# Optimization experiments

Measured on AMD Instinct MI355X. Metric: run time of the kernel, lower is better.

The kernel has to match this reference:

```python
import jax, jax.numpy as jnp
import numpy as np

B = 32; SEQ = 900; GRID = 30; PFX = 16; D = 512
H = 8; HD = 64; WS = 3; SS = 1
NW = (GRID // WS) ** 2; N = WS * WS
INTER = 1536  # find_multiple(round(4.0*512*2/3), 256)
EPS = 1e-5
SCALE = HD ** -0.5


def _rel_pos_index():
    coords = np.stack(np.meshgrid(np.arange(WS), np.arange(WS), indexing='ij')).reshape(2, -1)
    rel = (coords[:, :, None] - coords[:, None, :]).transpose(1, 2, 0).copy()
    rel[:, :, 0] += WS - 1
    rel[:, :, 1] += WS - 1
    rel[:, :, 0] *= 2 * WS - 1
    return rel.sum(-1)  # [N, N]


def _attn_mask():
    img = np.zeros((GRID, GRID))
    cnt = 0
    sl = (slice(0, -WS), slice(-WS, -SS), slice(-SS, None))
    for h in sl:
        for w in sl:
            img[h, w] = cnt
            cnt += 1
    mw = img.reshape(GRID // WS, WS, GRID // WS, WS).transpose(0, 2, 1, 3).reshape(-1, N)
    diff = mw[:, None, :] - mw[:, :, None]
    return np.where(diff != 0, -100.0, 0.0).astype(np.float32)  # [nW, N, N]


REL_IDX = _rel_pos_index()
MASK = _attn_mask()


def rms_norm(x):
    xf = x.astype(jnp.float32)
    v = jnp.mean(xf * xf, -1, keepdims=True)
    return (xf * jax.lax.rsqrt(v + EPS)).astype(x.dtype)


def swiglu(x, gu_w, down_w):
    gu = x @ gu_w.T
    gate, up = gu[..., :INTER], gu[..., INTER:]
    return (jax.nn.silu(gate) * up) @ down_w.T


def setup_inputs() -> dict:
    key = jax.random.key(0)
    ks = jax.random.split(key, 8)
    s = 0.02
    return {
        'hidden_states': jax.random.normal(ks[0], (B, PFX + SEQ, D), jnp.float32),
        'qkv_w': jax.random.normal(ks[1], (3 * D, D), jnp.float32) * s,
        'qkv_b': jnp.zeros((3 * D,), jnp.float32),
        'proj_w': jax.random.normal(ks[2], (D, D), jnp.float32) * s,
        'proj_b': jnp.zeros((D,), jnp.float32),
        'rel_bias': jax.random.normal(ks[3], ((2 * WS - 1) ** 2, H), jnp.float32) * s,
        'gu_w': jax.random.normal(ks[4], (2 * INTER, D), jnp.float32) * s,
        'down_w': jax.random.normal(ks[5], (D, INTER), jnp.float32) * s,
        'pgu_w': jax.random.normal(ks[6], (2 * INTER, D), jnp.float32) * s,
        'pdown_w': jax.random.normal(ks[7], (D, INTER), jnp.float32) * s,
    }


def reference(hidden_states, qkv_w, qkv_b, proj_w, proj_b, rel_bias, gu_w, down_w, pgu_w, pdown_w):
    hs = hidden_states
    prefix = hs[:, :PFX]                                     # [B, 16, D]
    grid = hs[:, PFX:] + jnp.mean(prefix, 1, keepdims=True)  # broadcast prefix mean
    x = grid.reshape(B, GRID, GRID, D)
    residual = x
    # cyclic shift
    x = jnp.roll(x, (-SS, -SS), (1, 2))
    # window partition -> [B*nW, N, D]
    xw = x.reshape(B, GRID // WS, WS, GRID // WS, WS, D).transpose(0, 1, 3, 2, 4, 5).reshape(B * NW, N, D)
    qkv = (xw @ qkv_w.T + qkv_b).reshape(B * NW, N, 3, H, HD).transpose(2, 0, 3, 1, 4)
    q, k, v = qkv[0] * SCALE, qkv[1], qkv[2]                 # [B*nW, H, N, HD]
    attn = jnp.einsum('whid,whjd->whij', q, k)
    bias = rel_bias[jnp.asarray(REL_IDX).reshape(-1)].reshape(N, N, H).transpose(2, 0, 1)
    attn = attn + bias[None]
    attn = attn.reshape(B, NW, H, N, N) + jnp.asarray(MASK)[None, :, None]
    attn = jax.nn.softmax(attn.reshape(B * NW, H, N, N), -1)
    out = jnp.einsum('whij,whjd->whid', attn, v).transpose(0, 2, 1, 3).reshape(B * NW, N, D)
    out = out @ proj_w.T + proj_b
    # window reverse + reverse shift
    x = out.reshape(B, GRID // WS, GRID // WS, WS, WS, D).transpose(0, 1, 3, 2, 4, 5).reshape(B, GRID, GRID, D)
    x = jnp.roll(x, (SS, SS), (1, 2))
    x = rms_norm(residual.reshape(B, SEQ, D) + x.reshape(B, SEQ, D))
    prefix = rms_norm(prefix + swiglu(prefix, pgu_w, pdown_w))
    hs = jnp.concatenate([prefix, x], 1)
    return rms_norm(hs + swiglu(hs, gu_w, down_w))
```

## Files before the change

### kernel.cpp

```cpp
#include <hip/hip_runtime.h>
#include <cstdint>
#include <cstddef>

typedef float f32x4 __attribute__((ext_vector_type(4)));
typedef short s16x8 __attribute__((ext_vector_type(8)));
typedef short s16x4 __attribute__((ext_vector_type(4)));

#define DEV static __device__ __forceinline__

DEV float bf2f(short s) {
  union { unsigned u; float f; } c;
  c.u = ((unsigned)(unsigned short)s) << 16;
  return c.f;
}
DEV short f2bf(float f) {
  union { float f; unsigned u; } c;
  c.f = f;
  unsigned r = c.u + 0x7fffu + ((c.u >> 16) & 1u);
  return (short)(r >> 16);
}
DEV float wave_allsum(float v) {
#pragma unroll
  for (int off = 32; off > 0; off >>= 1) v += __shfl_xor(v, off, 64);
  return v;
}
DEV void gload_lds16(const void* g, void* l) {
  __builtin_amdgcn_global_load_lds(
      (const __attribute__((address_space(1))) void*)g,
      (__attribute__((address_space(3))) void*)l, 16, 0, 0);
}
DEV float silu_f(float g) { return g / (1.f + __expf(-g)); }

DEV int xcd_swizzle(int orig, int nwg) {
  int q = nwg >> 3, r = nwg & 7;
  int xcd = orig & 7, pos = orig >> 3;
  return (xcd < r ? xcd * (q + 1) : r * (q + 1) + (xcd - r) * q) + pos;
}

DEV void sync_phase() {
  asm volatile("s_waitcnt vmcnt(0)" ::: "memory");
  __builtin_amdgcn_s_barrier();
  __builtin_amdgcn_sched_barrier(0);
}

enum { EPI_BF16 = 0, EPI_BIAS_BF16 = 1, EPI_SCATTER = 4, EPI_ADDOUT = 5, EPI_GU = 6 };

template <int EPI>
__global__ __launch_bounds__(512, 2) void gemm8(
    const short* __restrict__ A, const short* __restrict__ W,
    const float* __restrict__ bias, void* __restrict__ outp,
    int M, int N, int K)
{
  __shared__ short lds[65536];
  const int tid = threadIdx.x;
  const int wid = tid >> 6, lane = tid & 63;
  const int wr = wid >> 2, wc = wid & 3;
  const int nwg = gridDim.x * gridDim.y;
  const int orig = blockIdx.y * gridDim.x + blockIdx.x;
  const int wg = xcd_swizzle(orig, nwg);
  const int bx = wg % gridDim.x, by = wg / gridDim.x;
  const int row0 = by * 256;
  const int c0 = bx * 256;

  f32x4 acc[8][4];
#pragma unroll
  for (int m = 0; m < 8; ++m)
#pragma unroll
    for (int n = 0; n < 4; ++n) acc[m][n] = f32x4{0.f, 0.f, 0.f, 0.f};

  const int srow = tid >> 3;
  const int k8s = (tid & 7) ^ (srow & 7);
  const short* aub[4];
  const short* bub[4];
#pragma unroll
  for (int u = 0; u < 4; ++u) {
    aub[u] = A + (size_t)(row0 + u * 64 + srow) * K + k8s * 8;
    bub[u] = W + (size_t)(c0 + u * 64 + srow) * K + k8s * 8;
  }
  const int ldw = wid * 512;

#define SA(d, u, kt) gload_lds16(aub[u] + (kt), &lds[(d)*16384 + (u)*4096 + ldw])
#define SB(d, u, kt) gload_lds16(bub[u] + (kt), &lds[32768 + (d)*16384 + (u)*4096 + ldw])
#define GATE(VN)                                              \
  asm volatile("s_waitcnt vmcnt(" #VN ")" ::: "memory");      \
  __builtin_amdgcn_s_barrier();                               \
  __builtin_amdgcn_sched_barrier(0);

  const int kg0 = (lane >> 4) ^ (lane & 7);
  const int kg1 = (4 + (lane >> 4)) ^ (lane & 7);
  const int aoff = (wr * 128 + (lane & 15)) * 64;
  const int boff = 32768 + (wc * 64 + (lane & 15)) * 64;

#define READ_B(d)                                                              \
  _Pragma("unroll") for (int n = 0; n < 4; ++n) {                              \
    bfr[0][n] = *(const s16x8*)&lds[(d)*16384 + boff + n * 1024 + kg0 * 8];    \
    bfr[1][n] = *(const s16x8*)&lds[(d)*16384 + boff + n * 1024 + kg1 * 8];    \
  }
#define DO_PHASE(d, p)                                                         \
  do {                                                                         \
    s16x8 a00 = *(const s16x8*)&lds[(d)*16384 + aoff + (2*(p))*1024 + kg0*8];  \
    s16x8 a01 = *(const s16x8*)&lds[(d)*16384 + aoff + (2*(p))*1024 + kg1*8];  \
    s16x8 a10 = *(const s16x8*)&lds[(d)*16384 + aoff + (2*(p)+1)*1024 + kg0*8];\
    s16x8 a11 = *(const s16x8*)&lds[(d)*16384 + aoff + (2*(p)+1)*1024 + kg1*8];\
    __builtin_amdgcn_s_setprio(1);                                             \
    _Pragma("unroll") for (int n = 0; n < 4; ++n)                              \
      acc[2*(p)][n] = __builtin_amdgcn_mfma_f32_16x16x32_bf16(a00, bfr[0][n], acc[2*(p)][n], 0, 0, 0); \
    _Pragma("unroll") for (int n = 0; n < 4; ++n)                              \
      acc[2*(p)+1][n] = __builtin_amdgcn_mfma_f32_16x16x32_bf16(a10, bfr[0][n], acc[2*(p)+1][n], 0, 0, 0); \
    _Pragma("unroll") for (int n = 0; n < 4; ++n)                              \
      acc[2*(p)][n] = __builtin_amdgcn_mfma_f32_16x16x32_bf16(a01, bfr[1][n], acc[2*(p)][n], 0, 0, 0); \
    _Pragma("unroll") for (int n = 0; n < 4; ++n)                              \
      acc[2*(p)+1][n] = __builtin_amdgcn_mfma_f32_16x16x32_bf16(a11, bfr[1][n], acc[2*(p)+1][n], 0, 0, 0); \
    __builtin_amdgcn_s_setprio(0);                                             \
  } while (0)

  SB(0, 0, 0); SB(0, 1, 0); SB(0, 2, 0); SB(0, 3, 0);
  SA(0, 0, 0); SA(0, 2, 0); SA(0, 1, 0); SA(0, 3, 0);

  const int NT = K >> 6;
  for (int t = 0; t < NT - 1; ++t) {
    const int d = t & 1, d1 = d ^ 1;
    const int kn = (t + 1) * 64;
    s16x8 bfr[2][4];
    SB(d1, 0, kn); SB(d1, 1, kn);
    GATE(4);
    READ_B(d);
    DO_PHASE(d, 0);
    SB(d1, 2, kn); SB(d1, 3, kn);
    DO_PHASE(d, 1);
    SA(d1, 0, kn); SA(d1, 2, kn);
    GATE(6);
    DO_PHASE(d, 2);
    SA(d1, 1, kn); SA(d1, 3, kn);
    DO_PHASE(d, 3);
  }
  {
    const int d = (NT - 1) & 1;
    s16x8 bfr[2][4];
    GATE(2);
    READ_B(d);
    DO_PHASE(d, 0);
    DO_PHASE(d, 1);
    GATE(0);
    DO_PHASE(d, 2);
    DO_PHASE(d, 3);
  }
#undef SA
#undef SB
#undef READ_B
#undef DO_PHASE

  const int li = lane >> 4, lc = lane & 15;
#pragma unroll
  for (int m = 0; m < 8; ++m) {
#pragma unroll
    for (int i = 0; i < 4; ++i) {
      int gr = row0 + wr * 128 + m * 16 + li * 4 + i;
      if (gr >= M) continue;
      size_t orow;
      if (EPI == EPI_SCATTER) {
        int b = gr / 900, rem = gr % 900;
        int w = rem / 9, n_ = rem % 9;
        int wi = w / 10, wj = w % 10;
        int ii = n_ / 3, jj = n_ % 3;
        int gy = wi * 3 + ii + 1; if (gy >= 30) gy -= 30;
        int gx = wj * 3 + jj + 1; if (gx >= 30) gx -= 30;
        orow = (size_t)b * 900 + gy * 30 + gx;
      } else {
        orow = (size_t)gr;
      }
#pragma unroll
      for (int n = 0; n < 4; ++n) {
        int gc = c0 + wc * 64 + n * 16 + lc;
        float v = acc[m][n][i];
        if (EPI == EPI_BIAS_BF16 || EPI == EPI_SCATTER) v += bias[gc];
        if (EPI == EPI_ADDOUT) {
          float* po = (float*)outp;
          size_t oi = orow * (size_t)N + gc;
          po[oi] = po[oi] + v;
        } else {
          ((short*)outp)[orow * (size_t)N + gc] = f2bf(v);
        }
      }
    }
  }
}

__global__ __launch_bounds__(512, 2) void gemm8gu(
    const short* __restrict__ A, const short* __restrict__ Wg,
    const short* __restrict__ Wu, short* __restrict__ outp, int M, int K)
{
  __shared__ short lds[65536];
  const int tid = threadIdx.x;
  const int wid = tid >> 6, lane = tid & 63;
  const int wr = wid >> 1, wc = wid & 1;
  const int nwg = gridDim.x * gridDim.y;
  const int orig = blockIdx.y * gridDim.x + blockIdx.x;
  const int wg = xcd_swizzle(orig, nwg);
  const int bx = wg % gridDim.x, by = wg / gridDim.x;
  const int row0 = by * 256;
  const int colg = bx * 128;

  f32x4 accg[4][4], accu[4][4];
#pragma unroll
  for (int m = 0; m < 4; ++m)
#pragma unroll
    for (int n = 0; n < 4; ++n) {
      accg[m][n] = f32x4{0.f, 0.f, 0.f, 0.f};
      accu[m][n] = f32x4{0.f, 0.f, 0.f, 0.f};
    }

  const int srow = tid >> 3;
  const int k8s = (tid & 7) ^ (srow & 7);
  const short* aub[4];
  const short* bub[4];
#pragma unroll
  for (int u = 0; u < 4; ++u)
    aub[u] = A + (size_t)(row0 + u * 64 + srow) * K + k8s * 8;
#pragma unroll
  for (int u = 0; u < 2; ++u) {
    bub[u]     = Wg + (size_t)(colg + u * 64 + srow) * K + k8s * 8;
    bub[u + 2] = Wu + (size_t)(colg + u * 64 + srow) * K + k8s * 8;
  }
  const int ldw = wid * 512;

#define SA(d, u, kt) gload_lds16(aub[u] + (kt), &lds[(d)*16384 + (u)*4096 + ldw])
#define SB(d, u, kt) gload_lds16(bub[u] + (kt), &lds[32768 + (d)*16384 + (u)*4096 + ldw])

  const int kg0 = (lane >> 4) ^ (lane & 7);
  const int kg1 = (4 + (lane >> 4)) ^ (lane & 7);
  const int aoff = (wr * 64 + (lane & 15)) * 64;
  const int bgoff = 32768 + (wc * 64 + (lane & 15)) * 64;
  const int buoff = 32768 + (128 + wc * 64 + (lane & 15)) * 64;

#define READ_BF(d, BOFF)                                                       \
  _Pragma("unroll") for (int n = 0; n < 4; ++n) {                              \
    bfr[0][n] = *(const s16x8*)&lds[(d)*16384 + (BOFF) + n * 1024 + kg0 * 8];  \
    bfr[1][n] = *(const s16x8*)&lds[(d)*16384 + (BOFF) + n * 1024 + kg1 * 8];  \
  }
#define PHASE2(d, p, ACC)                                                      \
  do {                                                                         \
    s16x8 a00 = *(const s16x8*)&lds[(d)*16384 + aoff + (2*(p))*1024 + kg0*8];  \
    s16x8 a01 = *(const s16x8*)&lds[(d)*16384 + aoff + (2*(p))*1024 + kg1*8];  \
    s16x8 a10 = *(const s16x8*)&lds[(d)*16384 + aoff + (2*(p)+1)*1024 + kg0*8];\
    s16x8 a11 = *(const s16x8*)&lds[(d)*16384 + aoff + (2*(p)+1)*1024 + kg1*8];\
    __builtin_amdgcn_s_setprio(1);                                             \
    _Pragma("unroll") for (int n = 0; n < 4; ++n)                              \
      ACC[2*(p)][n] = __builtin_amdgcn_mfma_f32_16x16x32_bf16(a00, bfr[0][n], ACC[2*(p)][n], 0, 0, 0); \
    _Pragma("unroll") for (int n = 0; n < 4; ++n)                              \
      ACC[2*(p)+1][n] = __builtin_amdgcn_mfma_f32_16x16x32_bf16(a10, bfr[0][n], ACC[2*(p)+1][n], 0, 0, 0); \
    _Pragma("unroll") for (int n = 0; n < 4; ++n)                              \
      ACC[2*(p)][n] = __builtin_amdgcn_mfma_f32_16x16x32_bf16(a01, bfr[1][n], ACC[2*(p)][n], 0, 0, 0); \
    _Pragma("unroll") for (int n = 0; n < 4; ++n)                              \
      ACC[2*(p)+1][n] = __builtin_amdgcn_mfma_f32_16x16x32_bf16(a11, bfr[1][n], ACC[2*(p)+1][n], 0, 0, 0); \
    __builtin_amdgcn_s_setprio(0);                                             \
  } while (0)
#define GATE(VN)                                              \
  asm volatile("s_waitcnt vmcnt(" #VN ")" ::: "memory");      \
  __builtin_amdgcn_s_barrier();                               \
  __builtin_amdgcn_sched_barrier(0);

  SA(0, 0, 0); SA(0, 1, 0); SA(0, 2, 0); SA(0, 3, 0);
  SB(0, 0, 0); SB(0, 1, 0); SB(0, 2, 0); SB(0, 3, 0);

  const int NT = K >> 6;
  for (int t = 0; t < NT - 1; ++t) {
    const int d = t & 1, d1 = d ^ 1;
    const int kn = (t + 1) * 64;
    s16x8 bfr[2][4];
    GATE(2);
    READ_BF(d, bgoff);
    PHASE2(d, 0, accg);
    SA(d1, 0, kn); SA(d1, 1, kn);
    PHASE2(d, 1, accg);
    SA(d1, 2, kn); SA(d1, 3, kn);
    GATE(4);
    READ_BF(d, buoff);
    PHASE2(d, 0, accu);
    SB(d1, 0, kn); SB(d1, 1, kn);
    PHASE2(d, 1, accu);
    SB(d1, 2, kn); SB(d1, 3, kn);
  }
  {
    const int d = (NT - 1) & 1;
    s16x8 bfr[2][4];
    GATE(2);
    READ_BF(d, bgoff);
    PHASE2(d, 0, accg);
    PHASE2(d, 1, accg);
    GATE(0);
    READ_BF(d, buoff);
    PHASE2(d, 0, accu);
    PHASE2(d, 1, accu);
  }
#undef SA
#undef SB
#undef READ_BF
#undef PHASE2
#undef GATE

  const int li = lane >> 4, lc = lane & 15;
#pragma unroll
  for (int m = 0; m < 4; ++m) {
#pragma unroll
    for (int i = 0; i < 4; ++i) {
      int gr = row0 + wr * 64 + m * 16 + li * 4 + i;
      if (gr >= M) continue;
#pragma unroll
      for (int n = 0; n < 4; ++n) {
        int gc = colg + wc * 64 + n * 16 + lc;
        outp[(size_t)gr * 1536 + gc] = f2bf(silu_f(accg[m][n][i]) * accu[m][n][i]);
      }
    }
  }
}

template <int EPI>
__global__ __launch_bounds__(256) void gemm2(
    const short* __restrict__ A, const short* __restrict__ W,
    const short* __restrict__ Wu, const float* __restrict__ bias,
    void* __restrict__ outp, int M, int N, int K)
{
  __shared__ short As0[8192], Bs0[8192];
  __shared__ short As1[8192], Bs1[8192];
  const int tid = threadIdx.x;
  const int wave = tid >> 6, lane = tid & 63;
  const int nwg = gridDim.x * gridDim.y;
  const int orig = blockIdx.y * gridDim.x + blockIdx.x;
  const int wg = xcd_swizzle(orig, nwg);
  const int bx = wg % gridDim.x, by = wg / gridDim.x;
  const int row0 = by * 128;
  const int col0 = (EPI == EPI_GU) ? bx * 64 : bx * 128;
  const int wr = wave >> 1, wc = wave & 1;

  f32x4 acc[4][4];
#pragma unroll
  for (int m = 0; m < 4; ++m)
#pragma unroll
    for (int n = 0; n < 4; ++n) acc[m][n] = f32x4{0.f, 0.f, 0.f, 0.f};

  const short* aptr[4];
  const short* bptr[4];
  int ldst[4];
#pragma unroll
  for (int i = 0; i < 4; ++i) {
    int e = i * 2048 + tid * 8;
    int srow = e >> 6;
    int skg = ((e >> 3) & 7) ^ (srow & 7);
    aptr[i] = A + (size_t)(row0 + srow) * K + skg * 8;
    if (EPI == EPI_GU)
      bptr[i] = (srow < 64 ? W + (size_t)(col0 + srow) * K
                           : Wu + (size_t)(col0 + srow - 64) * K) + skg * 8;
    else
      bptr[i] = W + (size_t)(col0 + srow) * K + skg * 8;
    ldst[i] = i * 2048 + wave * 512;
  }

#define STAGE(AS, BS, KT)                                   \
  do {                                                      \
    _Pragma("unroll") for (int i = 0; i < 4; ++i)           \
        gload_lds16(aptr[i] + (KT), &AS[ldst[i]]);          \
    _Pragma("unroll") for (int i = 0; i < 4; ++i)           \
        gload_lds16(bptr[i] + (KT), &BS[ldst[i]]);          \
  } while (0)

#define COMPUTE(AS, BS)                                                        \
  do {                                                                         \
    _Pragma("unroll") for (int ks = 0; ks < 2; ++ks) {                         \
      s16x8 af[4], bfr[4];                                                     \
      _Pragma("unroll") for (int m = 0; m < 4; ++m) {                          \
        int row = wr * 64 + m * 16 + (lane & 15);                              \
        int kg = (ks * 4 + (lane >> 4)) ^ (row & 7);                           \
        af[m] = *(const s16x8*)&AS[row * 64 + kg * 8];                         \
      }                                                                        \
      _Pragma("unroll") for (int n = 0; n < 4; ++n) {                          \
        int brow = (EPI == EPI_GU)                                             \
                       ? ((n < 2 ? wc * 32 + n * 16                            \
                                 : 64 + wc * 32 + (n - 2) * 16) + (lane & 15)) \
                       : (wc * 64 + n * 16 + (lane & 15));                     \
        int kg = (ks * 4 + (lane >> 4)) ^ (brow & 7);                          \
        bfr[n] = *(const s16x8*)&BS[brow * 64 + kg * 8];                       \
      }                                                                        \
      _Pragma("unroll") for (int m = 0; m < 4; ++m)                            \
          _Pragma("unroll") for (int n = 0; n < 4; ++n)                        \
              acc[m][n] = __builtin_amdgcn_mfma_f32_16x16x32_bf16(             \
                  af[m], bfr[n], acc[m][n], 0, 0, 0);                          \
    }                                                                          \
  } while (0)

  STAGE(As0, Bs0, 0);
  sync_phase();
  for (int kt = 0; kt < K; kt += 128) {
    STAGE(As1, Bs1, kt + 64);
    COMPUTE(As0, Bs0);
    sync_phase();
    if (kt + 128 < K) STAGE(As0, Bs0, kt + 128);
    COMPUTE(As1, Bs1);
    if (kt + 128 < K) sync_phase();
  }
#undef STAGE
#undef COMPUTE

  const int lr = (lane >> 4) * 4, lc = lane & 15;
#pragma unroll
  for (int m = 0; m < 4; ++m) {
#pragma unroll
    for (int i = 0; i < 4; ++i) {
      int gr = row0 + wr * 64 + m * 16 + lr + i;
      if (EPI == EPI_GU) {
#pragma unroll
        for (int n = 0; n < 2; ++n) {
          int gc = col0 + wc * 32 + n * 16 + lc;
          float v = silu_f(acc[m][n][i]) * acc[m][n + 2][i];
          ((short*)outp)[(size_t)gr * N + gc] = f2bf(v);
        }
      } else {
#pragma unroll
        for (int n = 0; n < 4; ++n) {
          int gc = col0 + wc * 64 + n * 16 + lc;
          ((short*)outp)[(size_t)gr * N + gc] = f2bf(acc[m][n][i]);
        }
      }
    }
  }
}

__global__ __launch_bounds__(256) void cvt_all_kernel(
    const float* __restrict__ s_qkv, const float* __restrict__ s_proj,
    const float* __restrict__ s_gu, const float* __restrict__ s_down,
    const float* __restrict__ s_pgu, const float* __restrict__ s_pdown,
    short* __restrict__ dst) {
  int i = blockIdx.x * 256 + threadIdx.x;
  if (i >= 1441792) return;
  const float* src;
  int base;
  if (i < 262144) {
    if (i < 196608) { src = s_qkv; base = 0; }
    else            { src = s_proj; base = 196608; }
  } else if (i < 851968) {
    if (i < 655360) { src = s_gu; base = 262144; }
    else            { src = s_down; base = 655360; }
  } else {
    if (i < 1245184) { src = s_pgu; base = 851968; }
    else             { src = s_pdown; base = 1245184; }
  }
  f32x4 v = *(const f32x4*)(src + (size_t)(i - base) * 4);
  s16x4 o;
#pragma unroll
  for (int e = 0; e < 4; ++e) o[e] = f2bf(v[e]);
  *(s16x4*)(dst + (size_t)i * 4) = o;
}

__global__ __launch_bounds__(256) void prefix_cvt_kernel(const float* __restrict__ hs,
                                                         short* __restrict__ dst) {
  int i = blockIdx.x * 256 + threadIdx.x;
  if (i >= 512 * 128) return;
  int r = i >> 7, c4 = i & 127;
  int b = r >> 4, t = r & 15;
  f32x4 v = *(const f32x4*)(hs + ((size_t)b * 916 + t) * 512 + c4 * 4);
  s16x4 o;
#pragma unroll
  for (int e = 0; e < 4; ++e) o[e] = f2bf(v[e]);
  *(s16x4*)(dst + (size_t)r * 512 + c4 * 4) = o;
}

__global__ __launch_bounds__(512) void mean_kernel(const float* __restrict__ hs,
                                                   float* __restrict__ m) {
  int b = blockIdx.x, d = threadIdx.x;
  float s = 0.f;
#pragma unroll
  for (int t = 0; t < 16; ++t) s += hs[((size_t)b * 916 + t) * 512 + d];
  m[b * 512 + d] = s * (1.f / 16.f);
}

__global__ __launch_bounds__(256) void prep_kernel(const float* __restrict__ hs,
                                                   const float* __restrict__ m,
                                                   short* __restrict__ xw) {
  int idx = blockIdx.x * 256 + threadIdx.x;
  if (idx >= 32 * 900 * 128) return;
  int c4 = idx & 127;
  int row = idx >> 7;
  int b = row / 900, rem = row % 900;
  int gy = rem / 30, gx = rem % 30;
  f32x4 v = *(const f32x4*)(hs + ((size_t)b * 916 + 16 + rem) * 512 + c4 * 4);
  f32x4 mm = *(const f32x4*)(m + b * 512 + c4 * 4);
  v += mm;
  int ry = gy + 29; if (ry >= 30) ry -= 30;
  int rx = gx + 29; if (rx >= 30) rx -= 30;
  int wi = ry / 3, ii = ry % 3, wj = rx / 3, jj = rx % 3;
  size_t xrow = (size_t)((b * 100 + wi * 10 + wj) * 9 + ii * 3 + jj);
  s16x4 o;
#pragma unroll
  for (int e = 0; e < 4; ++e) o[e] = f2bf(v[e]);
  *(s16x4*)(xw + xrow * 512 + c4 * 4) = o;
}

__global__ __launch_bounds__(256) void attn_kernel(const short* __restrict__ qkv,
                                                   const float* __restrict__ rel_bias,
                                                   short* __restrict__ outp) {
  __shared__ short sq[9 * 512];
  __shared__ short sk[9 * 512];
  __shared__ short sv[9 * 512];
  __shared__ float sS[648];
  const int wlin = blockIdx.x;
  const int w = wlin % 100;
  const int wi = w / 10, wj = w % 10;
  const int tid = threadIdx.x;
  const short* base = qkv + (size_t)wlin * 9 * 1536;
  for (int idx = tid; idx < 1728; idx += 256) {
    int n = idx / 192, c8 = idx % 192;
    s16x8 v = *(const s16x8*)(base + (size_t)n * 1536 + c8 * 8);
    int which = c8 >> 6;
    short* dst = (which == 0) ? sq : (which == 1) ? sk : sv;
    *(s16x8*)(dst + n * 512 + (c8 & 63) * 8) = v;
  }
  __syncthreads();
  for (int idx = tid; idx < 648; idx += 256) {
    int h = idx / 81, r = idx % 81, i = r / 9, j = r % 9;
    const short* qp = sq + i * 512 + h * 64;
    const short* kp = sk + j * 512 + h * 64;
    float dot = 0.f;
#pragma unroll
    for (int c = 0; c < 8; ++c) {
      s16x8 qv = *(const s16x8*)(qp + c * 8);
      s16x8 kv = *(const s16x8*)(kp + c * 8);
#pragma unroll
      for (int e = 0; e < 8; ++e) dot += bf2f(qv[e]) * bf2f(kv[e]);
    }
    float s = dot * 0.125f;
    int ia = i / 3, ja = i % 3, ib = j / 3, jb = j % 3;
    s += rel_bias[(5 * (ia - ib + 2) + (ja - jb + 2)) * 8 + h];
    int ra = wi * 3 + ia, ca = wj * 3 + ja, rb = wi * 3 + ib, cb = wj * 3 + jb;
    int rga = (ra < 27) ? 0 : (ra < 29) ? 1 : 2;
    int cga = (ca < 27) ? 0 : (ca < 29) ? 1 : 2;
    int rgb = (rb < 27) ? 0 : (rb < 29) ? 1 : 2;
    int cgb = (cb < 27) ? 0 : (cb < 29) ? 1 : 2;
    if (rga * 3 + cga != rgb * 3 + cgb) s -= 100.f;
    sS[idx] = s;
  }
  __syncthreads();
  if (tid < 72) {
    float* row = sS + tid * 9;
    float mx = row[0];
#pragma unroll
    for (int j = 1; j < 9; ++j) mx = fmaxf(mx, row[j]);
    float e[9], sum = 0.f;
#pragma unroll
    for (int j = 0; j < 9; ++j) { e[j] = __expf(row[j] - mx); sum += e[j]; }
    float inv = 1.f / sum;
#pragma unroll
    for (int j = 0; j < 9; ++j) row[j] = e[j] * inv;
  }
  __syncthreads();
  for (int idx = tid; idx < 576; idx += 256) {
    int h = idx / 72, r = idx % 72, i = r / 8, d8 = r % 8;
    const float* p = sS + (h * 9 + i) * 9;
    float a[8] = {0, 0, 0, 0, 0, 0, 0, 0};
#pragma unroll
    for (int j = 0; j < 9; ++j) {
      float pj = p[j];
      s16x8 vv = *(const s16x8*)(sv + j * 512 + h * 64 + d8 * 8);
#pragma unroll
      for (int e = 0; e < 8; ++e) a[e] += pj * bf2f(vv[e]);
    }
    s16x8 o;
#pragma unroll
    for (int e = 0; e < 8; ++e) o[e] = f2bf(a[e]);
    *(s16x8*)(outp + ((size_t)wlin * 9 + i) * 512 + h * 64 + d8 * 8) = o;
  }
}

__global__ __launch_bounds__(64) void addnorm1_kernel(const short* __restrict__ xw,
                                                      const short* __restrict__ p,
                                                      float* __restrict__ out,
                                                      short* __restrict__ hsb) {
  int row = blockIdx.x, lane = threadIdx.x;
  int b_ = row / 900, rem = row % 900;
  int gy = rem / 30, gx = rem % 30;
  int ry = gy + 29; if (ry >= 30) ry -= 30;
  int rx = gx + 29; if (rx >= 30) rx -= 30;
  size_t xrow = (size_t)((b_ * 100 + (ry / 3) * 10 + rx / 3) * 9 + (ry % 3) * 3 + rx % 3);
  s16x8 a8 = *(const s16x8*)(xw + xrow * 512 + lane * 8);
  s16x8 b8 = *(const s16x8*)(p + (size_t)row * 512 + lane * 8);
  float x[8];
  float ss = 0.f;
#pragma unroll
  for (int e = 0; e < 8; ++e) {
    x[e] = bf2f(a8[e]) + bf2f(b8[e]);
    ss += x[e] * x[e];
  }
  ss = wave_allsum(ss);
  float sc = rsqrtf(ss * (1.f / 512.f) + 1e-5f);
  size_t orow = ((size_t)b_ * 916 + 16 + rem) * 512 + lane * 8;
  s16x8 o;
#pragma unroll
  for (int e = 0; e < 8; ++e) {
    x[e] *= sc;
    o[e] = f2bf(x[e]);
  }
  *(f32x4*)(out + orow) = f32x4{x[0], x[1], x[2], x[3]};
  *(f32x4*)(out + orow + 4) = f32x4{x[4], x[5], x[6], x[7]};
  *(s16x8*)(hsb + orow) = o;
}

__global__ __launch_bounds__(64) void prefix_addnorm_kernel(const float* __restrict__ hs,
                                                            const short* __restrict__ pd,
                                                            float* __restrict__ out,
                                                            short* __restrict__ hsb) {
  int r = blockIdx.x, lane = threadIdx.x;
  int b = r >> 4, t = r & 15;
  size_t orow = ((size_t)b * 916 + t) * 512;
  f32x4 x[2];
  float ss = 0.f;
#pragma unroll
  for (int i = 0; i < 2; ++i) {
    f32x4 a = *(const f32x4*)(hs + orow + i * 256 + lane * 4);
    s16x4 d = *(const s16x4*)(pd + (size_t)r * 512 + i * 256 + lane * 4);
#pragma unroll
    for (int e = 0; e < 4; ++e) a[e] += bf2f(d[e]);
    x[i] = a;
    ss += a[0] * a[0] + a[1] * a[1] + a[2] * a[2] + a[3] * a[3];
  }
  ss = wave_allsum(ss);
  float sc = rsqrtf(ss * (1.f / 512.f) + 1e-5f);
#pragma unroll
  for (int i = 0; i < 2; ++i) {
    f32x4 y = x[i] * sc;
    *(f32x4*)(out + orow + i * 256 + lane * 4) = y;
    s16x4 o;
#pragma unroll
    for (int e = 0; e < 4; ++e) o[e] = f2bf(y[e]);
    *(s16x4*)(hsb + orow + i * 256 + lane * 4) = o;
  }
}

__global__ __launch_bounds__(64) void final_addnorm_kernel(float* __restrict__ io) {
  int row = blockIdx.x, lane = threadIdx.x;
  size_t off = (size_t)row * 512;
  f32x4 x[2];
  float ss = 0.f;
#pragma unroll
  for (int i = 0; i < 2; ++i) {
    f32x4 a = *(const f32x4*)(io + off + i * 256 + lane * 4);
    x[i] = a;
    ss += a[0] * a[0] + a[1] * a[1] + a[2] * a[2] + a[3] * a[3];
  }
  ss = wave_allsum(ss);
  float sc = rsqrtf(ss * (1.f / 512.f) + 1e-5f);
#pragma unroll
  for (int i = 0; i < 2; ++i)
    *(f32x4*)(io + off + i * 256 + lane * 4) = x[i] * sc;
}

static constexpr size_t OFF_WQKV   = 0;
static constexpr size_t OFF_WPROJ  = 1572864;
static constexpr size_t OFF_WGU    = 2097152;
static constexpr size_t OFF_WDOWN  = 5242880;
static constexpr size_t OFF_WPGU   = 6815744;
static constexpr size_t OFF_WPDOWN = 9961472;
static constexpr size_t OFF_MEAN   = 11534336;
static constexpr size_t OFF_PREFB  = 11599872;
static constexpr size_t OFF_PINTER = 13697024;
static constexpr size_t OFF_PDOUT  = 15269888;
static constexpr size_t OFF_XW     = 16777216;
static constexpr size_t OFF_QKV    = 46399488;
static constexpr size_t OFF_ATTNO  = 134873088;
static constexpr size_t OFF_PROJS  = OFF_QKV;
static constexpr size_t OFF_INTER  = OFF_XW;
static constexpr size_t OFF_HSB    = 164364288;

extern "C" void kernel_launch(void* const* d_in, const int* in_sizes, int n_in,
                              void* d_out, int out_size, void* d_ws, size_t ws_size,
                              hipStream_t stream) {
  const float* hs      = (const float*)d_in[0];
  const float* qkv_w   = (const float*)d_in[1];
  const float* qkv_b   = (const float*)d_in[2];
  const float* proj_w  = (const float*)d_in[3];
  const float* proj_b  = (const float*)d_in[4];
  const float* rel_b   = (const float*)d_in[5];
  const float* gu_w    = (const float*)d_in[6];
  const float* down_w  = (const float*)d_in[7];
  const float* pgu_w   = (const float*)d_in[8];
  const float* pdown_w = (const float*)d_in[9];

  char* ws = (char*)d_ws;
  short* Wqkv   = (short*)(ws + OFF_WQKV);
  short* Wproj  = (short*)(ws + OFF_WPROJ);
  short* Wgu    = (short*)(ws + OFF_WGU);
  short* Wdown  = (short*)(ws + OFF_WDOWN);
  short* Wpgu   = (short*)(ws + OFF_WPGU);
  short* Wpdown = (short*)(ws + OFF_WPDOWN);
  float* meanb  = (float*)(ws + OFF_MEAN);
  short* prefb  = (short*)(ws + OFF_PREFB);
  short* pinter = (short*)(ws + OFF_PINTER);
  short* pdout  = (short*)(ws + OFF_PDOUT);
  short* xw     = (short*)(ws + OFF_XW);
  short* qkvb   = (short*)(ws + OFF_QKV);
  short* attno  = (short*)(ws + OFF_ATTNO);
  short* projs  = (short*)(ws + OFF_PROJS);
  short* interb = (short*)(ws + OFF_INTER);
  short* hsb    = (short*)(ws + OFF_HSB);
  float* outf   = (float*)d_out;

  cvt_all_kernel<<<5632, 256, 0, stream>>>(qkv_w, proj_w, gu_w, down_w,
                                           pgu_w, pdown_w, (short*)ws);
  prefix_cvt_kernel<<<256, 256, 0, stream>>>(hs, prefb);

  mean_kernel<<<32, 512, 0, stream>>>(hs, meanb);
  prep_kernel<<<14400, 256, 0, stream>>>(hs, meanb, xw);

  gemm8<EPI_BIAS_BF16><<<dim3(6, 113), 512, 0, stream>>>(
      xw, Wqkv, qkv_b, qkvb, 28800, 1536, 512);
  attn_kernel<<<3200, 256, 0, stream>>>(qkvb, rel_b, attno);

  gemm8<EPI_SCATTER><<<dim3(2, 113), 512, 0, stream>>>(
      attno, Wproj, proj_b, projs, 28800, 512, 512);
  addnorm1_kernel<<<28800, 64, 0, stream>>>(xw, projs, outf, hsb);

  gemm2<EPI_GU><<<dim3(24, 4), 256, 0, stream>>>(
      prefb, Wpgu, Wpgu + 1536 * 512, nullptr, pinter, 512, 1536, 512);
  gemm2<EPI_BF16><<<dim3(4, 4), 256, 0, stream>>>(
      pinter, Wpdown, nullptr, nullptr, pdout, 512, 512, 1536);
  prefix_addnorm_kernel<<<512, 64, 0, stream>>>(hs, pdout, outf, hsb);

  gemm8gu<<<dim3(12, 115), 512, 0, stream>>>(
      hsb, Wgu, Wgu + 1536 * 512, interb, 29312, 512);
  gemm8<EPI_ADDOUT><<<dim3(2, 115), 512, 0, stream>>>(
      interb, Wdown, nullptr, outf, 29312, 512, 1536);
  final_addnorm_kernel<<<29312, 64, 0, stream>>>(outf);

  (void)in_sizes; (void)n_in; (void)out_size; (void)ws_size;
}
```

Baseline: 441.3 us.

## Write down-proj output as bf16, add residual in norm kernel, batch rows per block

The down-projection GEMM stops doing a read-modify-write of the fp32 output and writes a bf16 buffer instead. The final norm kernel now adds that buffer to the residual. The three add-norm kernels now process four rows per 256-thread block with 8-element vector accesses, which cuts block count and launch overhead. The gate/up GEMM loads A fragments once per k-tile and shares them between the gate and up MFMAs, at the cost of more live registers. Rounding the down-projection output to bf16 before the residual add slightly changes numerics.

```diff
diff --git a/kernel.cpp b/kernel.cpp
--- a/kernel.cpp
+++ b/kernel.cpp
@@ -43,7 +43,7 @@
   __builtin_amdgcn_sched_barrier(0);
 }
 
-enum { EPI_BF16 = 0, EPI_BIAS_BF16 = 1, EPI_SCATTER = 4, EPI_ADDOUT = 5, EPI_GU = 6 };
+enum { EPI_BF16 = 0, EPI_BIAS_BF16 = 1, EPI_SCATTER = 4, EPI_GU = 6 };
 
 template <int EPI>
 __global__ __launch_bounds__(512, 2) void gemm8(
@@ -174,13 +174,7 @@
         int gc = c0 + wc * 64 + n * 16 + lc;
         float v = acc[m][n][i];
         if (EPI == EPI_BIAS_BF16 || EPI == EPI_SCATTER) v += bias[gc];
-        if (EPI == EPI_ADDOUT) {
-          float* po = (float*)outp;
-          size_t oi = orow * (size_t)N + gc;
-          po[oi] = po[oi] + v;
-        } else {
-          ((short*)outp)[orow * (size_t)N + gc] = f2bf(v);
-        }
+        ((short*)outp)[orow * (size_t)N + gc] = f2bf(v);
       }
     }
   }
@@ -226,6 +220,10 @@
 
 #define SA(d, u, kt) gload_lds16(aub[u] + (kt), &lds[(d)*16384 + (u)*4096 + ldw])
 #define SB(d, u, kt) gload_lds16(bub[u] + (kt), &lds[32768 + (d)*16384 + (u)*4096 + ldw])
+#define GATE(VN)                                              \
+  asm volatile("s_waitcnt vmcnt(" #VN ")" ::: "memory");      \
+  __builtin_amdgcn_s_barrier();                               \
+  __builtin_amdgcn_sched_barrier(0);
 
   const int kg0 = (lane >> 4) ^ (lane & 7);
   const int kg1 = (4 + (lane >> 4)) ^ (lane & 7);
@@ -233,32 +231,29 @@
   const int bgoff = 32768 + (wc * 64 + (lane & 15)) * 64;
   const int buoff = 32768 + (128 + wc * 64 + (lane & 15)) * 64;
 
-#define READ_BF(d, BOFF)                                                       \
+#define READ_BF(d, BOFF, BF)                                                   \
   _Pragma("unroll") for (int n = 0; n < 4; ++n) {                              \
-    bfr[0][n] = *(const s16x8*)&lds[(d)*16384 + (BOFF) + n * 1024 + kg0 * 8];  \
-    bfr[1][n] = *(const s16x8*)&lds[(d)*16384 + (BOFF) + n * 1024 + kg1 * 8];  \
-  }
-#define PHASE2(d, p, ACC)                                                      \
+    BF[0][n] = *(const s16x8*)&lds[(d)*16384 + (BOFF) + n * 1024 + kg0 * 8];   \
+    BF[1][n] = *(const s16x8*)&lds[(d)*16384 + (BOFF) + n * 1024 + kg1 * 8];   \
+  }
+#define READ_A(d)                                                              \
+  _Pragma("unroll") for (int m = 0; m < 4; ++m) {                              \
+    af[0][m] = *(const s16x8*)&lds[(d)*16384 + aoff + m * 1024 + kg0 * 8];     \
+    af[1][m] = *(const s16x8*)&lds[(d)*16384 + aoff + m * 1024 + kg1 * 8];     \
+  }
+#define MM2(BF, h, ACC)                                                        \
   do {                                                                         \
-    s16x8 a00 = *(const s16x8*)&lds[(d)*16384 + aoff + (2*(p))*1024 + kg0*8];  \
-    s16x8 a01 = *(const s16x8*)&lds[(d)*16384 + aoff + (2*(p))*1024 + kg1*8];  \
-    s16x8 a10 = *(const s16x8*)&lds[(d)*16384 + aoff + (2*(p)+1)*1024 + kg0*8];\
-    s16x8 a11 = *(const s16x8*)&lds[(d)*16384 + aoff + (2*(p)+1)*1024 + kg1*8];\
     __builtin_amdgcn_s_setprio(1);                                             \
     _Pragma("unroll") for (int n = 0; n < 4; ++n)                              \
-      ACC[2*(p)][n] = __builtin_amdgcn_mfma_f32_16x16x32_bf16(a00, bfr[0][n], ACC[2*(p)][n], 0, 0, 0); \
+      ACC[2*(h)][n] = __builtin_amdgcn_mfma_f32_16x16x32_bf16(af[0][2*(h)], BF[0][n], ACC[2*(h)][n], 0, 0, 0); \
     _Pragma("unroll") for (int n = 0; n < 4; ++n)                              \
-      ACC[2*(p)+1][n] = __builtin_amdgcn_mfma_f32_16x16x32_bf16(a10, bfr[0][n], ACC[2*(p)+1][n], 0, 0, 0); \
+      ACC[2*(h)+1][n] = __builtin_amdgcn_mfma_f32_16x16x32_bf16(af[0][2*(h)+1], BF[0][n], ACC[2*(h)+1][n], 0, 0, 0); \
     _Pragma("unroll") for (int n = 0; n < 4; ++n)                              \
-      ACC[2*(p)][n] = __builtin_amdgcn_mfma_f32_16x16x32_bf16(a01, bfr[1][n], ACC[2*(p)][n], 0, 0, 0); \
+      ACC[2*(h)][n] = __builtin_amdgcn_mfma_f32_16x16x32_bf16(af[1][2*(h)], BF[1][n], ACC[2*(h)][n], 0, 0, 0); \
     _Pragma("unroll") for (int n = 0; n < 4; ++n)                              \
-      ACC[2*(p)+1][n] = __builtin_amdgcn_mfma_f32_16x16x32_bf16(a11, bfr[1][n], ACC[2*(p)+1][n], 0, 0, 0); \
+      ACC[2*(h)+1][n] = __builtin_amdgcn_mfma_f32_16x16x32_bf16(af[1][2*(h)+1], BF[1][n], ACC[2*(h)+1][n], 0, 0, 0); \
     __builtin_amdgcn_s_setprio(0);                                             \
   } while (0)
-#define GATE(VN)                                              \
-  asm volatile("s_waitcnt vmcnt(" #VN ")" ::: "memory");      \
-  __builtin_amdgcn_s_barrier();                               \
-  __builtin_amdgcn_sched_barrier(0);
 
   SA(0, 0, 0); SA(0, 1, 0); SA(0, 2, 0); SA(0, 3, 0);
   SB(0, 0, 0); SB(0, 1, 0); SB(0, 2, 0); SB(0, 3, 0);
@@ -267,36 +262,39 @@
   for (int t = 0; t < NT - 1; ++t) {
     const int d = t & 1, d1 = d ^ 1;
     const int kn = (t + 1) * 64;
-    s16x8 bfr[2][4];
+    s16x8 af[2][4], bg[2][4], bu[2][4];
     GATE(2);
-    READ_BF(d, bgoff);
-    PHASE2(d, 0, accg);
+    READ_BF(d, bgoff, bg);
+    READ_A(d);
+    MM2(bg, 0, accg);
     SA(d1, 0, kn); SA(d1, 1, kn);
-    PHASE2(d, 1, accg);
+    MM2(bg, 1, accg);
     SA(d1, 2, kn); SA(d1, 3, kn);
     GATE(4);
-    READ_BF(d, buoff);
-    PHASE2(d, 0, accu);
+    READ_BF(d, buoff, bu);
+    MM2(bu, 0, accu);
     SB(d1, 0, kn); SB(d1, 1, kn);
-    PHASE2(d, 1, accu);
+    MM2(bu, 1, accu);
     SB(d1, 2, kn); SB(d1, 3, kn);
   }
   {
     const int d = (NT - 1) & 1;
-    s16x8 bfr[2][4];
+    s16x8 af[2][4], bg[2][4], bu[2][4];
     GATE(2);
-    READ_BF(d, bgoff);
-    PHASE2(d, 0, accg);
-    PHASE2(d, 1, accg);
+    READ_BF(d, bgoff, bg);
+    READ_A(d);
+    MM2(bg, 0, accg);
+    MM2(bg, 1, accg);
     GATE(0);
-    READ_BF(d, buoff);
-    PHASE2(d, 0, accu);
-    PHASE2(d, 1, accu);
+    READ_BF(d, buoff, bu);
+    MM2(bu, 0, accu);
+    MM2(bu, 1, accu);
   }
 #undef SA
 #undef SB
 #undef READ_BF
-#undef PHASE2
+#undef READ_A
+#undef MM2
 #undef GATE
 
   const int li = lane >> 4, lc = lane & 15;
@@ -570,11 +568,12 @@
   }
 }
 
-__global__ __launch_bounds__(64) void addnorm1_kernel(const short* __restrict__ xw,
-                                                      const short* __restrict__ p,
-                                                      float* __restrict__ out,
-                                                      short* __restrict__ hsb) {
-  int row = blockIdx.x, lane = threadIdx.x;
+__global__ __launch_bounds__(256) void addnorm1_kernel(const short* __restrict__ xw,
+                                                       const short* __restrict__ p,
+                                                       float* __restrict__ out,
+                                                       short* __restrict__ hsb) {
+  int row = blockIdx.x * 4 + (threadIdx.x >> 6);
+  int lane = threadIdx.x & 63;
   int b_ = row / 900, rem = row % 900;
   int gy = rem / 30, gx = rem % 30;
   int ry = gy + 29; if (ry >= 30) ry -= 30;
@@ -603,53 +602,58 @@
   *(s16x8*)(hsb + orow) = o;
 }
 
-__global__ __launch_bounds__(64) void prefix_addnorm_kernel(const float* __restrict__ hs,
-                                                            const short* __restrict__ pd,
-                                                            float* __restrict__ out,
-                                                            short* __restrict__ hsb) {
-  int r = blockIdx.x, lane = threadIdx.x;
+__global__ __launch_bounds__(256) void prefix_addnorm_kernel(const float* __restrict__ hs,
+                                                             const short* __restrict__ pd,
+                                                             float* __restrict__ out,
+                                                             short* __restrict__ hsb) {
+  int r = blockIdx.x * 4 + (threadIdx.x >> 6);
+  int lane = threadIdx.x & 63;
   int b = r >> 4, t = r & 15;
-  size_t orow = ((size_t)b * 916 + t) * 512;
-  f32x4 x[2];
+  size_t orow = ((size_t)b * 916 + t) * 512 + lane * 8;
+  f32x4 a0 = *(const f32x4*)(hs + orow);
+  f32x4 a1 = *(const f32x4*)(hs + orow + 4);
+  s16x8 d8 = *(const s16x8*)(pd + (size_t)r * 512 + lane * 8);
+  float x[8];
   float ss = 0.f;
 #pragma unroll
-  for (int i = 0; i < 2; ++i) {
-    f32x4 a = *(const f32x4*)(hs + orow + i * 256 + lane * 4);
-    s16x4 d = *(const s16x4*)(pd + (size_t)r * 512 + i * 256 + lane * 4);
-#pragma unroll
-    for (int e = 0; e < 4; ++e) a[e] += bf2f(d[e]);
-    x[i] = a;
-    ss += a[0] * a[0] + a[1] * a[1] + a[2] * a[2] + a[3] * a[3];
+  for (int e = 0; e < 8; ++e) {
+    x[e] = (e < 4 ? a0[e] : a1[e - 4]) + bf2f(d8[e]);
+    ss += x[e] * x[e];
   }
   ss = wave_allsum(ss);
   float sc = rsqrtf(ss * (1.f / 512.f) + 1e-5f);
-#pragma unroll
-  for (int i = 0; i < 2; ++i) {
-    f32x4 y = x[i] * sc;
-    *(f32x4*)(out + orow + i * 256 + lane * 4) = y;
-    s16x4 o;
-#pragma unroll
-    for (int e = 0; e < 4; ++e) o[e] = f2bf(y[e]);
-    *(s16x4*)(hsb + orow + i * 256 + lane * 4) = o;
-  }
-}
-
-__global__ __launch_bounds__(64) void final_addnorm_kernel(float* __restrict__ io) {
-  int row = blockIdx.x, lane = threadIdx.x;
-  size_t off = (size_t)row * 512;
-  f32x4 x[2];
+  s16x8 o;
+#pragma unroll
+  for (int e = 0; e < 8; ++e) {
+    x[e] *= sc;
+    o[e] = f2bf(x[e]);
+  }
+  *(f32x4*)(out + orow) = f32x4{x[0], x[1], x[2], x[3]};
+  *(f32x4*)(out + orow + 4) = f32x4{x[4], x[5], x[6], x[7]};
+  *(s16x8*)(hsb + orow) = o;
+}
+
+__global__ __launch_bounds__(256) void final_addnorm_kernel(const short* __restrict__ dn,
+                                                            float* __restrict__ io) {
+  int row = blockIdx.x * 4 + (threadIdx.x >> 6);
+  int lane = threadIdx.x & 63;
+  size_t off = (size_t)row * 512 + lane * 8;
+  f32x4 a0 = *(const f32x4*)(io + off);
+  f32x4 a1 = *(const f32x4*)(io + off + 4);
+  s16x8 d8 = *(const s16x8*)(dn + off);
+  float x[8];
   float ss = 0.f;
 #pragma unroll
-  for (int i = 0; i < 2; ++i) {
-    f32x4 a = *(const f32x4*)(io + off + i * 256 + lane * 4);
-    x[i] = a;
-    ss += a[0] * a[0] + a[1] * a[1] + a[2] * a[2] + a[3] * a[3];
+  for (int e = 0; e < 8; ++e) {
+    x[e] = (e < 4 ? a0[e] : a1[e - 4]) + bf2f(d8[e]);
+    ss += x[e] * x[e];
   }
   ss = wave_allsum(ss);
   float sc = rsqrtf(ss * (1.f / 512.f) + 1e-5f);
 #pragma unroll
-  for (int i = 0; i < 2; ++i)
-    *(f32x4*)(io + off + i * 256 + lane * 4) = x[i] * sc;
+  for (int e = 0; e < 8; ++e) x[e] *= sc;
+  *(f32x4*)(io + off) = f32x4{x[0], x[1], x[2], x[3]};
+  *(f32x4*)(io + off + 4) = f32x4{x[4], x[5], x[6], x[7]};
 }
 
 static constexpr size_t OFF_WQKV   = 0;
@@ -668,6 +672,7 @@
 static constexpr size_t OFF_PROJS  = OFF_QKV;
 static constexpr size_t OFF_INTER  = OFF_XW;
 static constexpr size_t OFF_HSB    = 164364288;
+static constexpr size_t OFF_DNOUT  = OFF_ATTNO;
 
 extern "C" void kernel_launch(void* const* d_in, const int* in_sizes, int n_in,
                               void* d_out, int out_size, void* d_ws, size_t ws_size,
@@ -700,6 +705,7 @@
   short* projs  = (short*)(ws + OFF_PROJS);
   short* interb = (short*)(ws + OFF_INTER);
   short* hsb    = (short*)(ws + OFF_HSB);
+  short* dnout  = (short*)(ws + OFF_DNOUT);
   float* outf   = (float*)d_out;
 
   cvt_all_kernel<<<5632, 256, 0, stream>>>(qkv_w, proj_w, gu_w, down_w,
@@ -715,19 +721,19 @@
 
   gemm8<EPI_SCATTER><<<dim3(2, 113), 512, 0, stream>>>(
       attno, Wproj, proj_b, projs, 28800, 512, 512);
-  addnorm1_kernel<<<28800, 64, 0, stream>>>(xw, projs, outf, hsb);
+  addnorm1_kernel<<<7200, 256, 0, stream>>>(xw, projs, outf, hsb);
 
   gemm2<EPI_GU><<<dim3(24, 4), 256, 0, stream>>>(
       prefb, Wpgu, Wpgu + 1536 * 512, nullptr, pinter, 512, 1536, 512);
   gemm2<EPI_BF16><<<dim3(4, 4), 256, 0, stream>>>(
       pinter, Wpdown, nullptr, nullptr, pdout, 512, 512, 1536);
-  prefix_addnorm_kernel<<<512, 64, 0, stream>>>(hs, pdout, outf, hsb);
+  prefix_addnorm_kernel<<<128, 256, 0, stream>>>(hs, pdout, outf, hsb);
 
   gemm8gu<<<dim3(12, 115), 512, 0, stream>>>(
       hsb, Wgu, Wgu + 1536 * 512, interb, 29312, 512);
-  gemm8<EPI_ADDOUT><<<dim3(2, 115), 512, 0, stream>>>(
-      interb, Wdown, nullptr, outf, 29312, 512, 1536);
-  final_addnorm_kernel<<<29312, 64, 0, stream>>>(outf);
+  gemm8<EPI_BF16><<<dim3(2, 115), 512, 0, stream>>>(
+      interb, Wdown, nullptr, dnout, 29312, 512, 1536);
+  final_addnorm_kernel<<<7328, 256, 0, stream>>>(dnout, outf);
 
   (void)in_sizes; (void)n_in; (void)out_size; (void)ws_size;
 }
```

After: 425.7 us. 1.04x faster.
